# Kernel optimization log

Hardware: AMD Instinct MI355X
Metric: run time of the kernel (lower is better)

## Reference

```python
import jax, jax.numpy as jnp
import numpy as np

HEAD_SIZE = 64

def setup_inputs() -> dict:
    key = jax.random.key(0)
    ks = jax.random.split(key, 5)
    B, T, C, H = 4, 4096, 1024, HEAD_SIZE
    scale = 1.0 / np.sqrt(C)
    return {
        "x": jax.random.normal(ks[0], (B, T, C), dtype=jnp.float32),
        "Wq": jax.random.normal(ks[1], (C, H), dtype=jnp.float32) * scale,
        "Wk": jax.random.normal(ks[2], (C, H), dtype=jnp.float32) * scale,
        "Wv": jax.random.normal(ks[3], (C, H), dtype=jnp.float32) * scale,
        "decay": jnp.full((1,), -0.8, dtype=jnp.float32),
    }

def reference(x, Wq, Wk, Wv, decay):
    # x: [B,T,C]; Wq/Wk/Wv: [C,H]; decay: [1]
    B, T, C = x.shape
    H = Wq.shape[1]
    q = jnp.einsum('btc,ch->bth', x, Wq)
    k = jnp.einsum('btc,ch->bth', x, Wk)
    v = jnp.einsum('btc,ch->bth', x, Wv)
    wei = jnp.einsum('bth,bsh->bts', q, k) * (H ** -0.5)  # [B,T,T]
    idx = jnp.arange(T)
    dist = jnp.minimum(idx[None, :] - idx[:, None], 0).astype(x.dtype)  # j - i, clamped max 0
    ripple_bias = dist * jnp.abs(decay[0])
    wei = wei + ripple_bias
    causal = idx[None, :] <= idx[:, None]  # lower-triangular True
    wei = jnp.where(causal, wei, -jnp.inf)
    wei = jax.nn.softmax(wei, axis=-1)
    # dropout p=0.0 -> identity (inference)
    return jnp.einsum('bts,bsh->bth', wei, v)
```

## Files before the change

kernel.cpp:

```cpp
#include <hip/hip_runtime.h>
#include <math.h>

#define BB 4
#define TT 4096
#define CC 1024
#define HH 64
#define MM (BB*TT)

typedef __attribute__((ext_vector_type(8))) short  short8;
typedef __attribute__((ext_vector_type(4))) short  short4v;
typedef __attribute__((ext_vector_type(4))) float  f32x4;

typedef const __attribute__((address_space(1))) unsigned int GU;
typedef __attribute__((address_space(3))) unsigned int LU;

static __device__ __forceinline__ unsigned short f2bf(float f) {
    union { float f; unsigned u; } v; v.f = f;
    unsigned r = v.u + 0x7FFF + ((v.u >> 16) & 1);
    return (unsigned short)(r >> 16);
}

__global__ __launch_bounds__(256) void convw_kernel(
        const float* __restrict__ Wq, const float* __restrict__ Wk,
        const float* __restrict__ Wv, unsigned short* __restrict__ wtb) {
    __shared__ unsigned short sW[64][66];
    const int m    = blockIdx.x >> 4;
    const int cblk = blockIdx.x & 15;
    const float* W = (m == 0) ? Wq : (m == 1) ? Wk : Wv;
    const int lane = threadIdx.x & 63;
    const int w    = threadIdx.x >> 6;
    #pragma unroll
    for (int rep = 0; rep < 16; ++rep) {
        const int cl = w * 16 + rep;
        sW[cl][lane] = f2bf(W[(size_t)(cblk * 64 + cl) * HH + lane]);
    }
    __syncthreads();
    #pragma unroll
    for (int rep = 0; rep < 16; ++rep) {
        const int h2 = w * 16 + rep;
        wtb[(size_t)(m * 64 + h2) * CC + cblk * 64 + lane] = sW[lane][h2];
    }
}

__global__ __launch_bounds__(256, 4) void gemm_kernel(
        const float* __restrict__ x,
        const unsigned short* __restrict__ wtb,
        unsigned short* __restrict__ qb,
        unsigned short* __restrict__ kb,
        unsigned short* __restrict__ vt) {
    __shared__ unsigned short As[32 * 64];
    __shared__ unsigned short Bs[192 * 64];

    const int t    = threadIdx.x;
    const int lane = t & 63;
    const int w    = t >> 6;
    const int l15  = lane & 15;
    const int lg   = lane >> 4;
    const int row0 = blockIdx.x * 32;
    const int rg   = (w >> 1) * 16;
    const int wc   = (w & 1) * 96;

    f32x4 acc[6];
    #pragma unroll
    for (int j = 0; j < 6; ++j) acc[j] = (f32x4){0.f, 0.f, 0.f, 0.f};

    const int ar  = t >> 3;
    const int akq = t & 7;
    const float* xrow = x + (size_t)(row0 + ar) * CC + akq * 8;
    char* adst = (char*)As + ar * 128 + ((akq ^ (ar & 7)) * 16);

    float4 a0 = *reinterpret_cast<const float4*>(xrow);
    float4 a1 = *reinterpret_cast<const float4*>(xrow + 4);

    for (int kc = 0; kc < CC; kc += 64) {
        short8 av;
        av[0] = (short)f2bf(a0.x); av[1] = (short)f2bf(a0.y);
        av[2] = (short)f2bf(a0.z); av[3] = (short)f2bf(a0.w);
        av[4] = (short)f2bf(a1.x); av[5] = (short)f2bf(a1.y);
        av[6] = (short)f2bf(a1.z); av[7] = (short)f2bf(a1.w);
        *reinterpret_cast<short8*>(adst) = av;

        #pragma unroll
        for (int it = 0; it < 6; ++it) {
            const int lidx = it * 4096 + t * 16;
            const int r  = lidx >> 7;
            const int cb = (((lidx & 127) >> 4) ^ (r & 7));
            const unsigned short* g = wtb + (size_t)r * CC + kc + cb * 8;
            __builtin_amdgcn_global_load_lds((GU*)g,
                (LU*)((char*)Bs + it * 4096 + w * 1024), 16, 0, 0);
        }
        __syncthreads();

        if (kc + 64 < CC) {
            a0 = *reinterpret_cast<const float4*>(xrow + kc + 64);
            a1 = *reinterpret_cast<const float4*>(xrow + kc + 68);
        }

        const char* Asc = (const char*)As;
        const char* Bsc = (const char*)Bs;
        const int swz = (l15 & 7) << 4;

        short8 af[2];
        #pragma unroll
        for (int kh = 0; kh < 2; ++kh) {
            const int r = rg + l15;
            af[kh] = *(const short8*)(Asc + r * 128 + ((kh * 64 + lg * 16) ^ swz));
        }
        #pragma unroll
        for (int kh = 0; kh < 2; ++kh)
            #pragma unroll
            for (int nf = 0; nf < 6; ++nf) {
                const int n = wc + nf * 16 + l15;
                short8 bf = *(const short8*)(Bsc + n * 128 + ((kh * 64 + lg * 16) ^ swz));
                acc[nf] = __builtin_amdgcn_mfma_f32_16x16x32_bf16(
                    af[kh], bf, acc[nf], 0, 0, 0);
            }
        __syncthreads();
    }

    const int b = row0 >> 12;
    #pragma unroll
    for (int nf = 0; nf < 6; ++nf) {
        const int ng = wc + nf * 16 + l15;
        const int m  = ng >> 6, h = ng & 63;
        const int rowbase = row0 + rg + lg * 4;
        if (m == 2) {
            short4v pk;
            pk[0] = (short)f2bf(acc[nf][0]);
            pk[1] = (short)f2bf(acc[nf][1]);
            pk[2] = (short)f2bf(acc[nf][2]);
            pk[3] = (short)f2bf(acc[nf][3]);
            *reinterpret_cast<short4v*>(
                &vt[((size_t)(b * 64 + h)) * TT + (rowbase & (TT - 1))]) = pk;
        } else {
            unsigned short* dst = (m == 0) ? qb : kb;
            #pragma unroll
            for (int r = 0; r < 4; ++r)
                dst[(size_t)(rowbase + r) * HH + h] = f2bf(acc[nf][r]);
        }
    }
}

__global__ __launch_bounds__(256) void attn_kernel(
        const unsigned short* __restrict__ qb,
        const unsigned short* __restrict__ kb,
        const unsigned short* __restrict__ vt,
        const float* __restrict__ decay,
        float* __restrict__ out) {
    __shared__ unsigned short P[4][16 * 168];

    const int lane = threadIdx.x & 63;
    const int w    = threadIdx.x >> 6;
    const int l15  = lane & 15;
    const int lg   = lane >> 4;
    const int qt   = blockIdx.x * 4 + w;
    const int gb   = qt >> 8;
    const int i0   = (qt & 255) << 4;

    const float dec = fabsf(decay[0]);
    const size_t bbase = (size_t)gb * TT;

    short8 af0, af1;
    {
        const unsigned short* qp = qb + (bbase + i0 + l15) * HH + lg * 8;
        af0 = *(const short8*)(qp);
        af1 = *(const short8*)(qp + 32);
    }

    float psum[4] = {0.f, 0.f, 0.f, 0.f};
    unsigned short* Pw = &P[w][0];

    if (i0 >= 144) {
        const int js = i0 - 144;
        const unsigned short* kp = kb + (bbase + js + l15) * HH + lg * 8;
        #pragma unroll
        for (int ts = 0; ts < 10; ++ts) {
            short8 b0 = *(const short8*)(kp + (size_t)ts * 16 * HH);
            short8 b1 = *(const short8*)(kp + (size_t)ts * 16 * HH + 32);
            f32x4 s = (f32x4){0.f, 0.f, 0.f, 0.f};
            s = __builtin_amdgcn_mfma_f32_16x16x32_bf16(af0, b0, s, 0, 0, 0);
            s = __builtin_amdgcn_mfma_f32_16x16x32_bf16(af1, b1, s, 0, 0, 0);
            const int d0 = 144 + lg * 4 - ts * 16 - l15;
            #pragma unroll
            for (int r = 0; r < 4; ++r) {
                const int d = d0 + r;
                float sv = s[r] * 0.125f - dec * (float)d - 12.0f;
                float p  = (ts == 9 && d < 0) ? 0.0f : __expf(sv);
                psum[r] += p;
                Pw[(lg * 4 + r) * 168 + ts * 16 + l15] = f2bf(p);
            }
        }
        #pragma unroll
        for (int off = 1; off < 16; off <<= 1)
            #pragma unroll
            for (int r = 0; r < 4; ++r)
                psum[r] += __shfl_xor(psum[r], off, 64);

        asm volatile("s_waitcnt lgkmcnt(0)" ::: "memory");
        __builtin_amdgcn_sched_barrier(0);

        f32x4 oacc[4];
        #pragma unroll
        for (int ht = 0; ht < 4; ++ht) oacc[ht] = (f32x4){0.f, 0.f, 0.f, 0.f};
        const unsigned short* vp = vt + ((size_t)(gb * 64) + l15) * TT + js + lg * 8;

        __builtin_amdgcn_s_setprio(1);
        #pragma unroll
        for (int kt = 0; kt < 5; ++kt) {
            short8 pa = *(const short8*)((const char*)Pw + l15 * 336 + kt * 64 + lg * 16);
            #pragma unroll
            for (int ht = 0; ht < 4; ++ht) {
                short8 bv = *(const short8*)(vp + (size_t)ht * 16 * TT + kt * 32);
                oacc[ht] = __builtin_amdgcn_mfma_f32_16x16x32_bf16(pa, bv, oacc[ht], 0, 0, 0);
            }
        }
        __builtin_amdgcn_s_setprio(0);

        float inv[4];
        #pragma unroll
        for (int r = 0; r < 4; ++r) inv[r] = 1.0f / psum[r];
        float* op = out + (bbase + i0 + lg * 4) * HH + l15;
        #pragma unroll
        for (int ht = 0; ht < 4; ++ht)
            #pragma unroll
            for (int r = 0; r < 4; ++r)
                op[(size_t)r * HH + ht * 16] = oacc[ht][r] * inv[r];
    } else {
        const int NS = (i0 >> 4) + 1;
        const int NK = (NS + 1) >> 1;
        const int dbase = i0 + lg * 4 - l15;
        const unsigned short* kp = kb + (bbase + l15) * HH + lg * 8;

        for (int ts = 0; ts < NS; ++ts) {
            short8 b0 = *(const short8*)(kp);
            short8 b1 = *(const short8*)(kp + 32);
            kp += 16 * HH;
            f32x4 s = (f32x4){0.f, 0.f, 0.f, 0.f};
            s = __builtin_amdgcn_mfma_f32_16x16x32_bf16(af0, b0, s, 0, 0, 0);
            s = __builtin_amdgcn_mfma_f32_16x16x32_bf16(af1, b1, s, 0, 0, 0);
            const int d0 = dbase - ts * 16;
            #pragma unroll
            for (int r = 0; r < 4; ++r) {
                const int d = d0 + r;
                float sv = s[r] * 0.125f - dec * (float)d - 12.0f;
                float p  = (d < 0) ? 0.0f : __expf(sv);
                psum[r] += p;
                Pw[(lg * 4 + r) * 168 + ts * 16 + l15] = f2bf(p);
            }
        }
        if (NS & 1) {
            #pragma unroll
            for (int r = 0; r < 4; ++r)
                Pw[(lg * 4 + r) * 168 + NS * 16 + l15] = 0;
        }
        #pragma unroll
        for (int off = 1; off < 16; off <<= 1)
            #pragma unroll
            for (int r = 0; r < 4; ++r)
                psum[r] += __shfl_xor(psum[r], off, 64);

        asm volatile("s_waitcnt lgkmcnt(0)" ::: "memory");
        __builtin_amdgcn_sched_barrier(0);

        f32x4 oacc[4];
        #pragma unroll
        for (int ht = 0; ht < 4; ++ht) oacc[ht] = (f32x4){0.f, 0.f, 0.f, 0.f};
        const unsigned short* vp = vt + ((size_t)(gb * 64) + l15) * TT + lg * 8;

        for (int kt = 0; kt < NK; ++kt) {
            short8 pa = *(const short8*)((const char*)Pw + l15 * 336 + kt * 64 + lg * 16);
            #pragma unroll
            for (int ht = 0; ht < 4; ++ht) {
                short8 bv = *(const short8*)(vp + (size_t)ht * 16 * TT + kt * 32);
                oacc[ht] = __builtin_amdgcn_mfma_f32_16x16x32_bf16(pa, bv, oacc[ht], 0, 0, 0);
            }
        }

        float inv[4];
        #pragma unroll
        for (int r = 0; r < 4; ++r) inv[r] = 1.0f / psum[r];
        float* op = out + (bbase + i0 + lg * 4) * HH + l15;
        #pragma unroll
        for (int ht = 0; ht < 4; ++ht)
            #pragma unroll
            for (int r = 0; r < 4; ++r)
                op[(size_t)r * HH + ht * 16] = oacc[ht][r] * inv[r];
    }
}

extern "C" void kernel_launch(void* const* d_in, const int* in_sizes, int n_in,
                              void* d_out, int out_size, void* d_ws, size_t ws_size,
                              hipStream_t stream) {
    const float* x     = (const float*)d_in[0];
    const float* Wq    = (const float*)d_in[1];
    const float* Wk    = (const float*)d_in[2];
    const float* Wv    = (const float*)d_in[3];
    const float* decay = (const float*)d_in[4];
    float* out = (float*)d_out;

    unsigned short* qb  = (unsigned short*)d_ws;
    unsigned short* kb  = qb + (size_t)MM * HH;
    unsigned short* vt  = kb + (size_t)MM * HH;
    unsigned short* wtb = vt + (size_t)MM * HH;

    convw_kernel<<<48, 256, 0, stream>>>(Wq, Wk, Wv, wtb);
    gemm_kernel<<<MM / 32, 256, 0, stream>>>(x, wtb, qb, kb, vt);
    attn_kernel<<<MM / 64, 256, 0, stream>>>(qb, kb, vt, decay, out);
}
```

Before: 41.03 us.

## Double-buffer weight tiles and load x directly into registers in QKV GEMM

Rewrites the projection GEMM to use 512 threads with 8 waves, each computing 16x48 outputs. The weight tile is double-buffered in shared memory with prefetch of the next K-chunk. The activation fragment is loaded straight from global memory into MFMA registers, which removes the A-tile staging through LDS. Explicit vmcnt waits and raw barriers let the next tile load overlap the current compute, at the cost of larger LDS usage and reliance on exact counts of in-flight memory operations.

```diff
diff --git a/kernel.cpp b/kernel.cpp
--- a/kernel.cpp
+++ b/kernel.cpp
@@ -42,85 +42,108 @@
     }
 }
 
-__global__ __launch_bounds__(256, 4) void gemm_kernel(
+__global__ __launch_bounds__(512, 4) void gemm_kernel(
         const float* __restrict__ x,
         const unsigned short* __restrict__ wtb,
         unsigned short* __restrict__ qb,
         unsigned short* __restrict__ kb,
         unsigned short* __restrict__ vt) {
-    __shared__ unsigned short As[32 * 64];
-    __shared__ unsigned short Bs[192 * 64];
-
-    const int t    = threadIdx.x;
-    const int lane = t & 63;
-    const int w    = t >> 6;
+    __shared__ unsigned short Bs[2][192 * 64];
+
+    const int tid  = threadIdx.x;
+    const int lane = tid & 63;
+    const int w    = tid >> 6;
     const int l15  = lane & 15;
     const int lg   = lane >> 4;
     const int row0 = blockIdx.x * 32;
-    const int rg   = (w >> 1) * 16;
-    const int wc   = (w & 1) * 96;
-
-    f32x4 acc[6];
-    #pragma unroll
-    for (int j = 0; j < 6; ++j) acc[j] = (f32x4){0.f, 0.f, 0.f, 0.f};
-
-    const int ar  = t >> 3;
-    const int akq = t & 7;
-    const float* xrow = x + (size_t)(row0 + ar) * CC + akq * 8;
-    char* adst = (char*)As + ar * 128 + ((akq ^ (ar & 7)) * 16);
-
-    float4 a0 = *reinterpret_cast<const float4*>(xrow);
-    float4 a1 = *reinterpret_cast<const float4*>(xrow + 4);
-
-    for (int kc = 0; kc < CC; kc += 64) {
-        short8 av;
-        av[0] = (short)f2bf(a0.x); av[1] = (short)f2bf(a0.y);
-        av[2] = (short)f2bf(a0.z); av[3] = (short)f2bf(a0.w);
-        av[4] = (short)f2bf(a1.x); av[5] = (short)f2bf(a1.y);
-        av[6] = (short)f2bf(a1.z); av[7] = (short)f2bf(a1.w);
-        *reinterpret_cast<short8*>(adst) = av;
-
-        #pragma unroll
-        for (int it = 0; it < 6; ++it) {
-            const int lidx = it * 4096 + t * 16;
-            const int r  = lidx >> 7;
-            const int cb = (((lidx & 127) >> 4) ^ (r & 7));
-            const unsigned short* g = wtb + (size_t)r * CC + kc + cb * 8;
-            __builtin_amdgcn_global_load_lds((GU*)g,
-                (LU*)((char*)Bs + it * 4096 + w * 1024), 16, 0, 0);
-        }
-        __syncthreads();
-
-        if (kc + 64 < CC) {
-            a0 = *reinterpret_cast<const float4*>(xrow + kc + 64);
-            a1 = *reinterpret_cast<const float4*>(xrow + kc + 68);
-        }
-
-        const char* Asc = (const char*)As;
-        const char* Bsc = (const char*)Bs;
-        const int swz = (l15 & 7) << 4;
-
-        short8 af[2];
+    const int rg   = (w >> 2) * 16;
+    const int wc   = (w & 3) * 48;
+
+    f32x4 acc[3];
+    #pragma unroll
+    for (int j = 0; j < 3; ++j) acc[j] = (f32x4){0.f, 0.f, 0.f, 0.f};
+
+    const float* xrow = x + (size_t)(row0 + rg + l15) * CC + lg * 8;
+
+    #pragma unroll
+    for (int it = 0; it < 3; ++it) {
+        const int lidx = it * 8192 + tid * 16;
+        const int r  = lidx >> 7;
+        const int cb = (((lidx & 127) >> 4) ^ (r & 7));
+        const unsigned short* g = wtb + (size_t)r * CC + cb * 8;
+        __builtin_amdgcn_global_load_lds((GU*)g,
+            (LU*)((char*)Bs[0] + it * 8192 + w * 1024), 16, 0, 0);
+    }
+    float4 ac0 = *reinterpret_cast<const float4*>(xrow);
+    float4 ac1 = *reinterpret_cast<const float4*>(xrow + 4);
+    float4 ac2 = *reinterpret_cast<const float4*>(xrow + 32);
+    float4 ac3 = *reinterpret_cast<const float4*>(xrow + 36);
+    float4 an0, an1, an2, an3;
+
+    const int swz = (l15 & 7) << 4;
+
+    #pragma unroll
+    for (int t = 0; t < 16; ++t) {
+        if (t < 15) {
+            const int kcn = (t + 1) * 64;
+            char* bs = (char*)Bs[(t + 1) & 1];
+            #pragma unroll
+            for (int it = 0; it < 3; ++it) {
+                const int lidx = it * 8192 + tid * 16;
+                const int r  = lidx >> 7;
+                const int cb = (((lidx & 127) >> 4) ^ (r & 7));
+                const unsigned short* g = wtb + (size_t)r * CC + kcn + cb * 8;
+                __builtin_amdgcn_global_load_lds((GU*)g,
+                    (LU*)(bs + it * 8192 + w * 1024), 16, 0, 0);
+            }
+            an0 = *reinterpret_cast<const float4*>(xrow + kcn);
+            an1 = *reinterpret_cast<const float4*>(xrow + kcn + 4);
+            an2 = *reinterpret_cast<const float4*>(xrow + kcn + 32);
+            an3 = *reinterpret_cast<const float4*>(xrow + kcn + 36);
+            asm volatile("s_waitcnt vmcnt(7)" ::: "memory");
+        } else {
+            asm volatile("s_waitcnt vmcnt(0)" ::: "memory");
+        }
+        __builtin_amdgcn_s_barrier();
+
+        short8 af0, af1;
+        af0[0] = (short)f2bf(ac0.x); af0[1] = (short)f2bf(ac0.y);
+        af0[2] = (short)f2bf(ac0.z); af0[3] = (short)f2bf(ac0.w);
+        af0[4] = (short)f2bf(ac1.x); af0[5] = (short)f2bf(ac1.y);
+        af0[6] = (short)f2bf(ac1.z); af0[7] = (short)f2bf(ac1.w);
+        af1[0] = (short)f2bf(ac2.x); af1[1] = (short)f2bf(ac2.y);
+        af1[2] = (short)f2bf(ac2.z); af1[3] = (short)f2bf(ac2.w);
+        af1[4] = (short)f2bf(ac3.x); af1[5] = (short)f2bf(ac3.y);
+        af1[6] = (short)f2bf(ac3.z); af1[7] = (short)f2bf(ac3.w);
+
+        const char* Bsc = (const char*)Bs[t & 1];
+        short8 bf[3][2];
+        #pragma unroll
+        for (int nf = 0; nf < 3; ++nf)
+            #pragma unroll
+            for (int kh = 0; kh < 2; ++kh) {
+                const int n = wc + nf * 16 + l15;
+                bf[nf][kh] = *(const short8*)(Bsc + n * 128 + ((kh * 64 + lg * 16) ^ swz));
+            }
         #pragma unroll
         for (int kh = 0; kh < 2; ++kh) {
-            const int r = rg + l15;
-            af[kh] = *(const short8*)(Asc + r * 128 + ((kh * 64 + lg * 16) ^ swz));
-        }
-        #pragma unroll
-        for (int kh = 0; kh < 2; ++kh)
-            #pragma unroll
-            for (int nf = 0; nf < 6; ++nf) {
-                const int n = wc + nf * 16 + l15;
-                short8 bf = *(const short8*)(Bsc + n * 128 + ((kh * 64 + lg * 16) ^ swz));
+            short8 af = kh ? af1 : af0;
+            #pragma unroll
+            for (int nf = 0; nf < 3; ++nf)
                 acc[nf] = __builtin_amdgcn_mfma_f32_16x16x32_bf16(
-                    af[kh], bf, acc[nf], 0, 0, 0);
-            }
-        __syncthreads();
+                    af, bf[nf][kh], acc[nf], 0, 0, 0);
+        }
+
+        asm volatile("s_waitcnt lgkmcnt(0)" ::: "memory");
+        __builtin_amdgcn_sched_barrier(0);
+        __builtin_amdgcn_s_barrier();
+
+        ac0 = an0; ac1 = an1; ac2 = an2; ac3 = an3;
     }
 
     const int b = row0 >> 12;
     #pragma unroll
-    for (int nf = 0; nf < 6; ++nf) {
+    for (int nf = 0; nf < 3; ++nf) {
         const int ng = wc + nf * 16 + l15;
         const int m  = ng >> 6, h = ng & 63;
         const int rowbase = row0 + rg + lg * 4;
@@ -304,6 +327,6 @@
     unsigned short* wtb = vt + (size_t)MM * HH;
 
     convw_kernel<<<48, 256, 0, stream>>>(Wq, Wk, Wv, wtb);
-    gemm_kernel<<<MM / 32, 256, 0, stream>>>(x, wtb, qb, kb, vt);
+    gemm_kernel<<<MM / 32, 512, 0, stream>>>(x, wtb, qb, kb, vt);
     attn_kernel<<<MM / 64, 256, 0, stream>>>(qb, kb, vt, decay, out);
 }
```

Result: slower. 56.25 us (+37.1%).

## Enlarge QKV GEMM row tile and stage fp32 x via direct LDS loads

Applied to the files above, without the earlier changes.

The projection GEMM now processes 64 rows per block instead of 32, with each wave computing a 64x48 tile (4x3 MFMA fragments) rather than 16x96. That raises reuse of the weight tile loaded into LDS. The x tile is now brought into LDS as raw fp32 through global_load_lds with an XOR swizzle, and converted to bf16 at fragment-read time, replacing the register prefetch and convert path. The trade-offs are a larger LDS footprint, more registers, fewer blocks, a dropped occupancy hint, and repeated bf16 conversion of A per wave with no register prefetch overlap.

```diff
diff --git a/kernel.cpp b/kernel.cpp
--- a/kernel.cpp
+++ b/kernel.cpp
@@ -42,47 +42,46 @@
     }
 }
 
-__global__ __launch_bounds__(256, 4) void gemm_kernel(
+__global__ __launch_bounds__(256) void gemm_kernel(
         const float* __restrict__ x,
         const unsigned short* __restrict__ wtb,
         unsigned short* __restrict__ qb,
         unsigned short* __restrict__ kb,
         unsigned short* __restrict__ vt) {
-    __shared__ unsigned short As[32 * 64];
+    __shared__ float          As[64 * 64];
     __shared__ unsigned short Bs[192 * 64];
 
-    const int t    = threadIdx.x;
-    const int lane = t & 63;
-    const int w    = t >> 6;
+    const int tid  = threadIdx.x;
+    const int lane = tid & 63;
+    const int w    = tid >> 6;
     const int l15  = lane & 15;
     const int lg   = lane >> 4;
-    const int row0 = blockIdx.x * 32;
-    const int rg   = (w >> 1) * 16;
-    const int wc   = (w & 1) * 96;
-
-    f32x4 acc[6];
+    const int row0 = blockIdx.x * 64;
+
+    f32x4 acc[4][3];
     #pragma unroll
-    for (int j = 0; j < 6; ++j) acc[j] = (f32x4){0.f, 0.f, 0.f, 0.f};
-
-    const int ar  = t >> 3;
-    const int akq = t & 7;
-    const float* xrow = x + (size_t)(row0 + ar) * CC + akq * 8;
-    char* adst = (char*)As + ar * 128 + ((akq ^ (ar & 7)) * 16);
-
-    float4 a0 = *reinterpret_cast<const float4*>(xrow);
-    float4 a1 = *reinterpret_cast<const float4*>(xrow + 4);
+    for (int i = 0; i < 4; ++i)
+        #pragma unroll
+        for (int j = 0; j < 3; ++j)
+            acc[i][j] = (f32x4){0.f, 0.f, 0.f, 0.f};
+
+    const int arow_local = tid >> 4;
+    const int aslot      = (tid & 15) ^ arow_local;
+    const float* asrc0   = x + (size_t)(row0 + arow_local) * CC + aslot * 4;
+
+    const int bbyte0 = w * 1024 + lane * 16;
+    const int swz    = (l15 & 7) << 4;
 
     for (int kc = 0; kc < CC; kc += 64) {
-        short8 av;
-        av[0] = (short)f2bf(a0.x); av[1] = (short)f2bf(a0.y);
-        av[2] = (short)f2bf(a0.z); av[3] = (short)f2bf(a0.w);
-        av[4] = (short)f2bf(a1.x); av[5] = (short)f2bf(a1.y);
-        av[6] = (short)f2bf(a1.z); av[7] = (short)f2bf(a1.w);
-        *reinterpret_cast<short8*>(adst) = av;
-
+        #pragma unroll
+        for (int p = 0; p < 4; ++p) {
+            const float* g = asrc0 + (size_t)p * 16 * CC + kc;
+            __builtin_amdgcn_global_load_lds((GU*)g,
+                (LU*)((char*)As + p * 4096 + w * 1024), 16, 0, 0);
+        }
         #pragma unroll
         for (int it = 0; it < 6; ++it) {
-            const int lidx = it * 4096 + t * 16;
+            const int lidx = it * 4096 + bbyte0;
             const int r  = lidx >> 7;
             const int cb = (((lidx & 127) >> 4) ^ (r & 7));
             const unsigned short* g = wtb + (size_t)r * CC + kc + cb * 8;
@@ -91,54 +90,68 @@
         }
         __syncthreads();
 
-        if (kc + 64 < CC) {
-            a0 = *reinterpret_cast<const float4*>(xrow + kc + 64);
-            a1 = *reinterpret_cast<const float4*>(xrow + kc + 68);
-        }
-
         const char* Asc = (const char*)As;
         const char* Bsc = (const char*)Bs;
-        const int swz = (l15 & 7) << 4;
-
-        short8 af[2];
-        #pragma unroll
-        for (int kh = 0; kh < 2; ++kh) {
-            const int r = rg + l15;
-            af[kh] = *(const short8*)(Asc + r * 128 + ((kh * 64 + lg * 16) ^ swz));
-        }
+
+        short8 af[4][2];
+        #pragma unroll
+        for (int mf = 0; mf < 4; ++mf)
+            #pragma unroll
+            for (int kh = 0; kh < 2; ++kh) {
+                const int r    = mf * 16 + l15;
+                const int l16  = kh * 8 + lg * 2;
+                const int pos0 = l16 ^ l15;
+                const float4 lo = *(const float4*)(Asc + r * 256 + pos0 * 16);
+                const float4 hi = *(const float4*)(Asc + r * 256 + (pos0 ^ 1) * 16);
+                short8 a;
+                a[0] = (short)f2bf(lo.x); a[1] = (short)f2bf(lo.y);
+                a[2] = (short)f2bf(lo.z); a[3] = (short)f2bf(lo.w);
+                a[4] = (short)f2bf(hi.x); a[5] = (short)f2bf(hi.y);
+                a[6] = (short)f2bf(hi.z); a[7] = (short)f2bf(hi.w);
+                af[mf][kh] = a;
+            }
+        short8 bf[3][2];
+        #pragma unroll
+        for (int nf = 0; nf < 3; ++nf)
+            #pragma unroll
+            for (int kh = 0; kh < 2; ++kh) {
+                const int n = w * 48 + nf * 16 + l15;
+                bf[nf][kh] = *(const short8*)(Bsc + n * 128 + ((kh * 64 + lg * 16) ^ swz));
+            }
         #pragma unroll
         for (int kh = 0; kh < 2; ++kh)
             #pragma unroll
-            for (int nf = 0; nf < 6; ++nf) {
-                const int n = wc + nf * 16 + l15;
-                short8 bf = *(const short8*)(Bsc + n * 128 + ((kh * 64 + lg * 16) ^ swz));
-                acc[nf] = __builtin_amdgcn_mfma_f32_16x16x32_bf16(
-                    af[kh], bf, acc[nf], 0, 0, 0);
-            }
+            for (int mf = 0; mf < 4; ++mf)
+                #pragma unroll
+                for (int nf = 0; nf < 3; ++nf)
+                    acc[mf][nf] = __builtin_amdgcn_mfma_f32_16x16x32_bf16(
+                        af[mf][kh], bf[nf][kh], acc[mf][nf], 0, 0, 0);
         __syncthreads();
     }
 
     const int b = row0 >> 12;
     #pragma unroll
-    for (int nf = 0; nf < 6; ++nf) {
-        const int ng = wc + nf * 16 + l15;
-        const int m  = ng >> 6, h = ng & 63;
-        const int rowbase = row0 + rg + lg * 4;
-        if (m == 2) {
-            short4v pk;
-            pk[0] = (short)f2bf(acc[nf][0]);
-            pk[1] = (short)f2bf(acc[nf][1]);
-            pk[2] = (short)f2bf(acc[nf][2]);
-            pk[3] = (short)f2bf(acc[nf][3]);
-            *reinterpret_cast<short4v*>(
-                &vt[((size_t)(b * 64 + h)) * TT + (rowbase & (TT - 1))]) = pk;
-        } else {
-            unsigned short* dst = (m == 0) ? qb : kb;
-            #pragma unroll
-            for (int r = 0; r < 4; ++r)
-                dst[(size_t)(rowbase + r) * HH + h] = f2bf(acc[nf][r]);
-        }
-    }
+    for (int mf = 0; mf < 4; ++mf)
+        #pragma unroll
+        for (int nf = 0; nf < 3; ++nf) {
+            const int ng = w * 48 + nf * 16 + l15;
+            const int m  = ng >> 6, h = ng & 63;
+            const int rowbase = row0 + mf * 16 + lg * 4;
+            if (m == 2) {
+                short4v pk;
+                pk[0] = (short)f2bf(acc[mf][nf][0]);
+                pk[1] = (short)f2bf(acc[mf][nf][1]);
+                pk[2] = (short)f2bf(acc[mf][nf][2]);
+                pk[3] = (short)f2bf(acc[mf][nf][3]);
+                *reinterpret_cast<short4v*>(
+                    &vt[((size_t)(b * 64 + h)) * TT + (rowbase & (TT - 1))]) = pk;
+            } else {
+                unsigned short* dst = (m == 0) ? qb : kb;
+                #pragma unroll
+                for (int r = 0; r < 4; ++r)
+                    dst[(size_t)(rowbase + r) * HH + h] = f2bf(acc[mf][nf][r]);
+            }
+        }
 }
 
 __global__ __launch_bounds__(256) void attn_kernel(
@@ -304,6 +317,6 @@
     unsigned short* wtb = vt + (size_t)MM * HH;
 
     convw_kernel<<<48, 256, 0, stream>>>(Wq, Wk, Wv, wtb);
-    gemm_kernel<<<MM / 32, 256, 0, stream>>>(x, wtb, qb, kb, vt);
+    gemm_kernel<<<MM / 64, 256, 0, stream>>>(x, wtb, qb, kb, vt);
     attn_kernel<<<MM / 64, 256, 0, stream>>>(qb, kb, vt, decay, out);
 }
```

Measured after the change: 45.99 us. +12.1%, slower.

## Software-pipeline projection GEMM with register-prefetched A/B and LDS-staged V transpose

Applied to the files above, without the earlier changes.

Reworks the QKV projection GEMM into a fully unrolled, multi-stage register prefetch pipeline. A (fp32 x) fragments are loaded straight into registers in MFMA layout and converted with packed bf16 convert instructions, so the A LDS tile goes away. B tiles are double-buffered in registers and written to LDS with explicit waitcnt/barrier scheduling. The V output transpose is staged through LDS so each thread does one vectorized 16-byte store. Occupancy hint drops from 4 to 3 blocks per SM, and the hand-scheduled waitcnts add register pressure and correctness fragility.

```diff
diff --git a/kernel.cpp b/kernel.cpp
--- a/kernel.cpp
+++ b/kernel.cpp
@@ -11,13 +11,21 @@
 typedef __attribute__((ext_vector_type(4))) short  short4v;
 typedef __attribute__((ext_vector_type(4))) float  f32x4;
 
-typedef const __attribute__((address_space(1))) unsigned int GU;
-typedef __attribute__((address_space(3))) unsigned int LU;
-
 static __device__ __forceinline__ unsigned short f2bf(float f) {
     union { float f; unsigned u; } v; v.f = f;
     unsigned r = v.u + 0x7FFF + ((v.u >> 16) & 1);
     return (unsigned short)(r >> 16);
+}
+
+static __device__ __forceinline__ short8 cvt8(float4 lo, float4 hi) {
+    unsigned u0, u1, u2, u3;
+    asm("v_cvt_pk_bf16_f32 %0, %1, %2" : "=v"(u0) : "v"(lo.x), "v"(lo.y));
+    asm("v_cvt_pk_bf16_f32 %0, %1, %2" : "=v"(u1) : "v"(lo.z), "v"(lo.w));
+    asm("v_cvt_pk_bf16_f32 %0, %1, %2" : "=v"(u2) : "v"(hi.x), "v"(hi.y));
+    asm("v_cvt_pk_bf16_f32 %0, %1, %2" : "=v"(u3) : "v"(hi.z), "v"(hi.w));
+    union { unsigned u[4]; short8 s; } r;
+    r.u[0] = u0; r.u[1] = u1; r.u[2] = u2; r.u[3] = u3;
+    return r.s;
 }
 
 __global__ __launch_bounds__(256) void convw_kernel(
@@ -42,102 +50,139 @@
     }
 }
 
-__global__ __launch_bounds__(256, 4) void gemm_kernel(
+__global__ __launch_bounds__(256, 3) void gemm_kernel(
         const float* __restrict__ x,
         const unsigned short* __restrict__ wtb,
         unsigned short* __restrict__ qb,
         unsigned short* __restrict__ kb,
         unsigned short* __restrict__ vt) {
-    __shared__ unsigned short As[32 * 64];
     __shared__ unsigned short Bs[192 * 64];
-
-    const int t    = threadIdx.x;
-    const int lane = t & 63;
-    const int w    = t >> 6;
+    __shared__ float vstage[64][33];
+
+    const int tid  = threadIdx.x;
+    const int lane = tid & 63;
+    const int w    = tid >> 6;
     const int l15  = lane & 15;
     const int lg   = lane >> 4;
     const int row0 = blockIdx.x * 32;
-    const int rg   = (w >> 1) * 16;
+    const int rg   = w >> 1;
     const int wc   = (w & 1) * 96;
 
     f32x4 acc[6];
     #pragma unroll
     for (int j = 0; j < 6; ++j) acc[j] = (f32x4){0.f, 0.f, 0.f, 0.f};
 
-    const int ar  = t >> 3;
-    const int akq = t & 7;
-    const float* xrow = x + (size_t)(row0 + ar) * CC + akq * 8;
-    char* adst = (char*)As + ar * 128 + ((akq ^ (ar & 7)) * 16);
-
-    float4 a0 = *reinterpret_cast<const float4*>(xrow);
-    float4 a1 = *reinterpret_cast<const float4*>(xrow + 4);
-
-    for (int kc = 0; kc < CC; kc += 64) {
-        short8 av;
-        av[0] = (short)f2bf(a0.x); av[1] = (short)f2bf(a0.y);
-        av[2] = (short)f2bf(a0.z); av[3] = (short)f2bf(a0.w);
-        av[4] = (short)f2bf(a1.x); av[5] = (short)f2bf(a1.y);
-        av[6] = (short)f2bf(a1.z); av[7] = (short)f2bf(a1.w);
-        *reinterpret_cast<short8*>(adst) = av;
-
-        #pragma unroll
-        for (int it = 0; it < 6; ++it) {
-            const int lidx = it * 4096 + t * 16;
-            const int r  = lidx >> 7;
-            const int cb = (((lidx & 127) >> 4) ^ (r & 7));
-            const unsigned short* g = wtb + (size_t)r * CC + kc + cb * 8;
-            __builtin_amdgcn_global_load_lds((GU*)g,
-                (LU*)((char*)Bs + it * 4096 + w * 1024), 16, 0, 0);
-        }
-        __syncthreads();
-
-        if (kc + 64 < CC) {
-            a0 = *reinterpret_cast<const float4*>(xrow + kc + 64);
-            a1 = *reinterpret_cast<const float4*>(xrow + kc + 68);
-        }
-
-        const char* Asc = (const char*)As;
+    const float* xrow = x + (size_t)(row0 + rg * 16 + l15) * CC;
+    const int lg8 = lg * 8;
+
+    const int tr = tid >> 3;
+    const int cb = (tid & 7) ^ (tr & 7);
+    const unsigned short* bwp[6];
+    #pragma unroll
+    for (int it = 0; it < 6; ++it)
+        bwp[it] = wtb + (size_t)(it * 32 + tr) * CC + cb * 8;
+
+    float4 araw[3][4];
+    short8 breg[2][6];
+
+#define KS(s_) (((s_) < 16 ? (s_) : 15) * 64)
+#define LOAD_B(s_, p_) { \
+    _Pragma("unroll") \
+    for (int it = 0; it < 6; ++it) \
+        breg[p_][it] = *(const short8*)(bwp[it] + KS(s_)); }
+#define LOAD_A(s_, sl_) { \
+    araw[sl_][0] = *(const float4*)(xrow + KS(s_) + lg8); \
+    araw[sl_][1] = *(const float4*)(xrow + KS(s_) + lg8 + 4); \
+    araw[sl_][2] = *(const float4*)(xrow + KS(s_) + 32 + lg8); \
+    araw[sl_][3] = *(const float4*)(xrow + KS(s_) + 36 + lg8); }
+#define WRITE_B(p_) { \
+    _Pragma("unroll") \
+    for (int it = 0; it < 6; ++it) \
+        *(short8*)((char*)Bs + it * 4096 + tid * 16) = breg[p_][it]; }
+#define FENCE() __builtin_amdgcn_sched_barrier(0x38F)
+
+    LOAD_B(0, 0); FENCE();
+    LOAD_A(0, 0); FENCE();
+    LOAD_A(1, 1); FENCE();
+    LOAD_B(1, 1); FENCE();
+    LOAD_A(2, 2); FENCE();
+    asm volatile("s_waitcnt vmcnt(10)" ::: "memory");
+    WRITE_B(0);
+    asm volatile("s_waitcnt lgkmcnt(0)" ::: "memory");
+    __builtin_amdgcn_sched_barrier(0);
+    __builtin_amdgcn_s_barrier();
+
+    const int swz = (l15 & 7) << 4;
+
+    #pragma unroll
+    for (int t = 0; t < 16; ++t) {
+        short8 af0 = cvt8(araw[t % 3][0], araw[t % 3][1]);
+        short8 af1 = cvt8(araw[t % 3][2], araw[t % 3][3]);
+
+        LOAD_B(t + 2, t & 1); FENCE();
+        LOAD_A(t + 3, t % 3); FENCE();
+
         const char* Bsc = (const char*)Bs;
-        const int swz = (l15 & 7) << 4;
-
-        short8 af[2];
+        short8 bf[6][2];
+        #pragma unroll
+        for (int nf = 0; nf < 6; ++nf)
+            #pragma unroll
+            for (int kh = 0; kh < 2; ++kh) {
+                const int n = wc + nf * 16 + l15;
+                bf[nf][kh] = *(const short8*)(Bsc + n * 128 + ((kh * 64 + lg * 16) ^ swz));
+            }
         #pragma unroll
         for (int kh = 0; kh < 2; ++kh) {
-            const int r = rg + l15;
-            af[kh] = *(const short8*)(Asc + r * 128 + ((kh * 64 + lg * 16) ^ swz));
-        }
-        #pragma unroll
-        for (int kh = 0; kh < 2; ++kh)
-            #pragma unroll
-            for (int nf = 0; nf < 6; ++nf) {
-                const int n = wc + nf * 16 + l15;
-                short8 bf = *(const short8*)(Bsc + n * 128 + ((kh * 64 + lg * 16) ^ swz));
+            short8 af = kh ? af1 : af0;
+            #pragma unroll
+            for (int nf = 0; nf < 6; ++nf)
                 acc[nf] = __builtin_amdgcn_mfma_f32_16x16x32_bf16(
-                    af[kh], bf, acc[nf], 0, 0, 0);
-            }
-        __syncthreads();
-    }
+                    af, bf[nf][kh], acc[nf], 0, 0, 0);
+        }
+
+        asm volatile("s_waitcnt vmcnt(10)" ::: "memory");
+        asm volatile("s_waitcnt lgkmcnt(0)" ::: "memory");
+        __builtin_amdgcn_sched_barrier(0);
+        __builtin_amdgcn_s_barrier();
+
+        WRITE_B((t + 1) & 1);
+        asm volatile("s_waitcnt lgkmcnt(0)" ::: "memory");
+        __builtin_amdgcn_sched_barrier(0);
+        __builtin_amdgcn_s_barrier();
+    }
+#undef KS
+#undef LOAD_B
+#undef LOAD_A
+#undef WRITE_B
+#undef FENCE
 
     const int b = row0 >> 12;
     #pragma unroll
     for (int nf = 0; nf < 6; ++nf) {
         const int ng = wc + nf * 16 + l15;
-        const int m  = ng >> 6, h = ng & 63;
-        const int rowbase = row0 + rg + lg * 4;
-        if (m == 2) {
-            short4v pk;
-            pk[0] = (short)f2bf(acc[nf][0]);
-            pk[1] = (short)f2bf(acc[nf][1]);
-            pk[2] = (short)f2bf(acc[nf][2]);
-            pk[3] = (short)f2bf(acc[nf][3]);
-            *reinterpret_cast<short4v*>(
-                &vt[((size_t)(b * 64 + h)) * TT + (rowbase & (TT - 1))]) = pk;
+        const int mbase = row0 + rg * 16 + lg * 4;
+        if (ng < 128) {
+            unsigned short* dst = ((ng < 64) ? qb : kb);
+            const int h = ng & 63;
+            #pragma unroll
+            for (int r = 0; r < 4; ++r)
+                dst[(size_t)(mbase + r) * HH + h] = f2bf(acc[nf][r]);
         } else {
-            unsigned short* dst = (m == 0) ? qb : kb;
-            #pragma unroll
-            for (int r = 0; r < 4; ++r)
-                dst[(size_t)(rowbase + r) * HH + h] = f2bf(acc[nf][r]);
-        }
+            #pragma unroll
+            for (int r = 0; r < 4; ++r)
+                vstage[ng - 128][rg * 16 + lg * 4 + r] = acc[nf][r];
+        }
+    }
+    __syncthreads();
+    {
+        const int h  = tid >> 2;
+        const int mq = (tid & 3) * 8;
+        short8 o;
+        #pragma unroll
+        for (int j = 0; j < 8; ++j)
+            o[j] = (short)f2bf(vstage[h][mq + j]);
+        *reinterpret_cast<short8*>(
+            vt + ((size_t)(b * 64 + h)) * TT + (row0 & (TT - 1)) + mq) = o;
     }
 }
 
```

Result: slower. 42.79 us (+4.3%).
